# Kernel tuning notes

Measured on AMD Instinct MI355X. Metric: run time of the kernel, lower is better.

The kernel has to match this reference:

```python
import jax, jax.numpy as jnp
import numpy as np

GRID_MIN, GRID_MAX, GRID_SIZE = -4.0, 4.0, 12
BANDWIDTH = (GRID_MAX - GRID_MIN) / max(GRID_SIZE - 1, 1)  # 8/11


def setup_inputs() -> dict:
    key = jax.random.key(0)
    k1, k2, k3, k4 = jax.random.split(key, 4)
    B, I, O, G = 16384, 512, 512, GRID_SIZE
    x = jax.random.normal(k1, (B, I), dtype=jnp.float32)
    coeff = jax.random.normal(k2, (I, O, G), dtype=jnp.float32) * 0.05
    base_w = jax.random.normal(k3, (O, I), dtype=jnp.float32) * (1.0 / np.sqrt(I))
    base_b = jax.random.normal(k4, (O,), dtype=jnp.float32) * 0.01
    centers = jnp.linspace(GRID_MIN, GRID_MAX, G, dtype=jnp.float32)
    return {"x": x, "coeff": coeff, "base_w": base_w, "base_b": base_b, "centers": centers}


def reference(x, coeff, base_w, base_b, centers):
    # RBF basis: [B, I, G]
    diff = (x[..., None] - centers) / jnp.float32(BANDWIDTH)
    basis = jnp.exp(-0.5 * diff * diff)
    # spline contraction over in_dim and grid: [B, O]
    spline = jnp.einsum('big,iog->bo', basis, coeff)
    # residual base linear (torch Linear: x @ W^T + b)
    return spline + x @ base_w.T + base_b
```

## Files before the change

### kernel.cpp

```cpp
#include <hip/hip_runtime.h>
#include <hip/hip_bf16.h>


#define N_DIM 512
#define I_DIM 512
#define KTOT  6656
#define NSTEP 104

typedef short short8 __attribute__((ext_vector_type(8)));
typedef float f32x16 __attribute__((ext_vector_type(16)));
typedef unsigned int u32x4 __attribute__((ext_vector_type(4)));

#define CVTPK(dst, lo, hi) \
  asm("v_cvt_pk_bf16_f32 %0, %1, %2" : "=v"(dst) : "v"(lo), "v"(hi))

__device__ __forceinline__ unsigned short f2bf(float f) {
  union { float f; unsigned int u; } c; c.f = f;
  unsigned int r = (c.u + 0x7FFFu + ((c.u >> 16) & 1)) >> 16;
  return (unsigned short)r;
}

__global__ __launch_bounds__(256) void prep_w(const float* __restrict__ coeff,
                                              const float* __restrict__ base_w,
                                              unsigned short* __restrict__ Wb2) {
  int t = blockIdx.x * 256 + threadIdx.x;
  int e0 = (t & 1) * 4;
  int go = t >> 1;
  int o  = go & 511;
  int g  = go >> 9;
  int k4 = g * 8 + e0;
  int ic = k4 / 832;
  int rem = k4 - ic * 832;
  int slot = rem >> 6;
  int ii = rem & 63;
  int i = ic * 64 + ii;
  float v0, v1, v2, v3;
  if (slot == 0) {
    const float4 bw = *(const float4*)(base_w + (size_t)o * I_DIM + i);
    v0 = bw.x; v1 = bw.y; v2 = bw.z; v3 = bw.w;
  } else {
    int gg = slot - 1;
    const float* cp = coeff + (size_t)i * (N_DIM * 12) + o * 12 + gg;
    v0 = cp[0]; v1 = cp[6144]; v2 = cp[2 * 6144]; v3 = cp[3 * 6144];
  }
  ushort4 s;
  s.x = f2bf(v0); s.y = f2bf(v1); s.z = f2bf(v2); s.w = f2bf(v3);
  *(ushort4*)(Wb2 + (size_t)go * 8 + e0) = s;
}

__global__ __launch_bounds__(512, 2) void kan_gemm(const float* __restrict__ x,
                                                   const unsigned short* __restrict__ Wb2,
                                                   const float* __restrict__ bias,
                                                   float* __restrict__ out) {
  __shared__ unsigned short Asw[4 * 8 * 128 * 8];

  const int tid  = threadIdx.x;
  const int lane = tid & 63;
  const int wid  = tid >> 6;
  const int wm   = wid >> 2, wn = wid & 3;
  const int l31  = lane & 31, hl = lane >> 5;

  const int bid = blockIdx.x;
  const int xcd = bid & 7, jj = bid >> 3;
  const int cb  = xcd >> 2;
  const int rb  = jj * 4 + (xcd & 3);
  const int M0  = rb * 128;
  const int N0  = cb * 256;

  const int arow = tid & 127;
  const int kgp  = tid >> 7;
  const float* xg = x + (size_t)(M0 + arow) * I_DIM + kgp * 16;
  const int aoff0 = ((kgp * 2) * 128 + arow) * 16;
  const int aoff1 = ((kgp * 2 + 1) * 128 + arow) * 16;

  const char* Wb = (const char*)Wb2;
  int boff[4][2];
#pragma unroll
  for (int s = 0; s < 4; ++s)
#pragma unroll
    for (int fo = 0; fo < 2; ++fo)
      boff[s][fo] = (((s * 2 + hl) * 512) + N0 + wn * 64 + fo * 32 + l31) * 16;

  const int aBase = (hl * 128 + wm * 64 + l31) * 16;

  f32x16 acc[2][2];
#pragma unroll
  for (int i = 0; i < 2; ++i)
#pragma unroll
    for (int j = 0; j < 2; ++j)
#pragma unroll
      for (int r = 0; r < 16; ++r) acc[i][j][r] = 0.f;

  float bb[16], ff[16];
  float4 xh[4];
  int eslot = 0, cchunk = 0;
#pragma unroll
  for (int q = 0; q < 4; ++q) xh[q] = *(const float4*)(xg + q * 4);

  auto loadB = [&](short8 (&bv)[4][2], int tt) {
    const char* WbT = Wb + (size_t)tt * 65536;
#pragma unroll
    for (int s = 0; s < 4; ++s) {
      bv[s][0] = *(const short8*)(WbT + boff[s][0]);
      bv[s][1] = *(const short8*)(WbT + boff[s][1]);
    }
  };

  auto emitA = [&](char* pDst) {
    unsigned int w[8];
    if (eslot == 0) {
      float f[16];
#pragma unroll
      for (int q = 0; q < 4; ++q) {
        f[q*4+0] = xh[q].x; f[q*4+1] = xh[q].y; f[q*4+2] = xh[q].z; f[q*4+3] = xh[q].w;
      }
#pragma unroll
      for (int j = 0; j < 8; ++j) CVTPK(w[j], f[2*j], f[2*j+1]);
      *(u32x4*)(pDst + aoff0) = (u32x4){w[0], w[1], w[2], w[3]};
      *(u32x4*)(pDst + aoff1) = (u32x4){w[4], w[5], w[6], w[7]};
#pragma unroll
      for (int j = 0; j < 16; ++j) {
        float u = fmaf(f[j], 1.375f, 5.5f);
        bb[j] = exp2f(-0.72134752044448170f * u * u);
        ff[j] = exp2f(fmaf(u, 1.44269504088896340f, -0.72134752044448170f));
      }
    } else {
#pragma unroll
      for (int j = 0; j < 8; ++j) CVTPK(w[j], bb[2*j], bb[2*j+1]);
      *(u32x4*)(pDst + aoff0) = (u32x4){w[0], w[1], w[2], w[3]};
      *(u32x4*)(pDst + aoff1) = (u32x4){w[4], w[5], w[6], w[7]};
#pragma unroll
      for (int j = 0; j < 16; ++j) {
        bb[j] *= ff[j];
        ff[j] *= 0.36787944117144233f;
      }
    }
    if (eslot == 1 && cchunk < 7) {
      ++cchunk;
      const float* xn = xg + (size_t)cchunk * 64;
#pragma unroll
      for (int q = 0; q < 4; ++q) xh[q] = *(const float4*)(xn + q * 4);
    }
    eslot = (eslot == 12) ? 0 : eslot + 1;
  };

#define MFMA_CLUSTER(AV, BV)                                                         \
  _Pragma("unroll")                                                                  \
  for (int s = 0; s < 4; ++s) {                                                      \
    acc[0][0] = __builtin_amdgcn_mfma_f32_32x32x16_bf16(AV[s][0], BV[s][0], acc[0][0], 0, 0, 0); \
    acc[0][1] = __builtin_amdgcn_mfma_f32_32x32x16_bf16(AV[s][0], BV[s][1], acc[0][1], 0, 0, 0); \
    acc[1][0] = __builtin_amdgcn_mfma_f32_32x32x16_bf16(AV[s][1], BV[s][0], acc[1][0], 0, 0, 0); \
    acc[1][1] = __builtin_amdgcn_mfma_f32_32x32x16_bf16(AV[s][1], BV[s][1], acc[1][1], 0, 0, 0); \
  }

  auto stepBody = [&](int tt, int rdOff, int emOff,
                      short8 (&bvC)[4][2], short8 (&bvN)[4][2]) {
    if (tt < NSTEP - 1) loadB(bvN, tt + 1);
    const char* pA = (const char*)Asw + rdOff;
    short8 av[4][2];
#pragma unroll
    for (int s = 0; s < 4; ++s) {
      av[s][0] = *(const short8*)(pA + aBase + s * 4096);
      av[s][1] = *(const short8*)(pA + aBase + s * 4096 + 512);
    }
    if (tt < NSTEP - 2) emitA((char*)Asw + emOff);
    MFMA_CLUSTER(av, bvC);
  };

  short8 bvA[4][2], bvB[4][2];
  emitA((char*)Asw);
  emitA((char*)Asw + 16384);
  loadB(bvA, 0);
  asm volatile("s_waitcnt lgkmcnt(0)" ::: "memory");
  __builtin_amdgcn_s_barrier();

#pragma unroll 1
  for (int t = 0; t < NSTEP; t += 4) {
    stepBody(t,     0,     32768, bvA, bvB);
    stepBody(t + 1, 16384, 49152, bvB, bvA);
    asm volatile("s_waitcnt lgkmcnt(0)" ::: "memory");
    __builtin_amdgcn_s_barrier();
    stepBody(t + 2, 32768, 0,     bvA, bvB);
    stepBody(t + 3, 49152, 16384, bvB, bvA);
    asm volatile("s_waitcnt lgkmcnt(0)" ::: "memory");
    __builtin_amdgcn_s_barrier();
  }

  float bvv[2];
#pragma unroll
  for (int fo = 0; fo < 2; ++fo) bvv[fo] = bias[N0 + wn * 64 + fo * 32 + l31];
  const int rbase = 4 * hl;
#pragma unroll
  for (int fb = 0; fb < 2; ++fb) {
#pragma unroll
    for (int fo = 0; fo < 2; ++fo) {
      const size_t cix = (size_t)(N0 + wn * 64 + fo * 32 + l31);
#pragma unroll
      for (int r = 0; r < 16; ++r) {
        int row = M0 + wm * 64 + fb * 32 + (r & 3) + 8 * (r >> 2) + rbase;
        out[(size_t)row * N_DIM + cix] = acc[fb][fo][r] + bvv[fo];
      }
    }
  }
}

extern "C" void kernel_launch(void* const* d_in, const int* in_sizes, int n_in,
                              void* d_out, int out_size, void* d_ws, size_t ws_size,
                              hipStream_t stream) {
  const float* x      = (const float*)d_in[0];
  const float* coeff  = (const float*)d_in[1];
  const float* base_w = (const float*)d_in[2];
  const float* base_b = (const float*)d_in[3];
  unsigned short* Wb2 = (unsigned short*)d_ws;

  prep_w<<<3328, 256, 0, stream>>>(coeff, base_w, Wb2);
  kan_gemm<<<256, 512, 0, stream>>>(x, Wb2, base_b, (float*)d_out);
}
```

Measured before the change: 132.6 us.

## Warp-specialize GEMM into producer waves for RBF basis and consumer MFMA waves

Splits the eight waves per block into four producer waves, which compute the bf16 x and RBF basis tiles into a four-deep LDS ring, and four consumer waves, which run the MFMAs over all 128 rows with a 64-column slice each. The K step is halved to 32 (208 steps), so the weight-prep layout and the LDS footprint change to match. The intent is to overlap the exp-heavy basis generation with tensor-core work instead of interleaving both in every wave. The cost is that only half the waves issue MFMAs, there are twice as many barriers, and consumer waves hold more accumulators.

```diff
diff --git a/kernel.cpp b/kernel.cpp
--- a/kernel.cpp
+++ b/kernel.cpp
@@ -5,7 +5,7 @@
 #define N_DIM 512
 #define I_DIM 512
 #define KTOT  6656
-#define NSTEP 104
+#define NSTEP 208
 
 typedef short short8 __attribute__((ext_vector_type(8)));
 typedef float f32x16 __attribute__((ext_vector_type(16)));
@@ -29,11 +29,11 @@
   int o  = go & 511;
   int g  = go >> 9;
   int k4 = g * 8 + e0;
-  int ic = k4 / 832;
-  int rem = k4 - ic * 832;
-  int slot = rem >> 6;
-  int ii = rem & 63;
-  int i = ic * 64 + ii;
+  int ic = k4 / 416;
+  int rem = k4 - ic * 416;
+  int slot = rem >> 5;
+  int ii = rem & 31;
+  int i = ic * 32 + ii;
   float v0, v1, v2, v3;
   if (slot == 0) {
     const float4 bw = *(const float4*)(base_w + (size_t)o * I_DIM + i);
@@ -52,13 +52,13 @@
                                                    const unsigned short* __restrict__ Wb2,
                                                    const float* __restrict__ bias,
                                                    float* __restrict__ out) {
-  __shared__ unsigned short Asw[4 * 8 * 128 * 8];
+  __shared__ unsigned short Asw[4 * 4 * 128 * 8];
 
   const int tid  = threadIdx.x;
   const int lane = tid & 63;
   const int wid  = tid >> 6;
-  const int wm   = wid >> 2, wn = wid & 3;
   const int l31  = lane & 31, hl = lane >> 5;
+  const bool isCons = (wid >= 4);
 
   const int bid = blockIdx.x;
   const int xcd = bid & 7, jj = bid >> 3;
@@ -67,57 +67,31 @@
   const int M0  = rb * 128;
   const int N0  = cb * 256;
 
-  const int arow = tid & 127;
-  const int kgp  = tid >> 7;
-  const float* xg = x + (size_t)(M0 + arow) * I_DIM + kgp * 16;
-  const int aoff0 = ((kgp * 2) * 128 + arow) * 16;
-  const int aoff1 = ((kgp * 2 + 1) * 128 + arow) * 16;
-
   const char* Wb = (const char*)Wb2;
-  int boff[4][2];
-#pragma unroll
-  for (int s = 0; s < 4; ++s)
-#pragma unroll
-    for (int fo = 0; fo < 2; ++fo)
-      boff[s][fo] = (((s * 2 + hl) * 512) + N0 + wn * 64 + fo * 32 + l31) * 16;
-
-  const int aBase = (hl * 128 + wm * 64 + l31) * 16;
-
-  f32x16 acc[2][2];
-#pragma unroll
-  for (int i = 0; i < 2; ++i)
-#pragma unroll
-    for (int j = 0; j < 2; ++j)
-#pragma unroll
-      for (int r = 0; r < 16; ++r) acc[i][j][r] = 0.f;
-
+
+  const int pid  = (wid & 3) * 64 + lane;
+  const int prow = pid & 127;
+  const int pkh  = pid >> 7;
+  const float* xrow = x + (size_t)(M0 + prow) * I_DIM + pkh * 16;
+  const int paoff0 = ((pkh * 2) * 128 + prow) * 16;
+  const int paoff1 = ((pkh * 2 + 1) * 128 + prow) * 16;
   float bb[16], ff[16];
-  float4 xh[4];
-  int eslot = 0, cchunk = 0;
-#pragma unroll
-  for (int q = 0; q < 4; ++q) xh[q] = *(const float4*)(xg + q * 4);
-
-  auto loadB = [&](short8 (&bv)[4][2], int tt) {
-    const char* WbT = Wb + (size_t)tt * 65536;
-#pragma unroll
-    for (int s = 0; s < 4; ++s) {
-      bv[s][0] = *(const short8*)(WbT + boff[s][0]);
-      bv[s][1] = *(const short8*)(WbT + boff[s][1]);
-    }
-  };
-
-  auto emitA = [&](char* pDst) {
+  int eslot = 0, echunk = 0;
+
+  auto emitP = [&](char* pDst) {
     unsigned int w[8];
     if (eslot == 0) {
-      float f[16];
-#pragma unroll
-      for (int q = 0; q < 4; ++q) {
-        f[q*4+0] = xh[q].x; f[q*4+1] = xh[q].y; f[q*4+2] = xh[q].z; f[q*4+3] = xh[q].w;
-      }
+      const float* xp = xrow + echunk * 32;
+      float4 p0 = *(const float4*)(xp);
+      float4 p1 = *(const float4*)(xp + 4);
+      float4 p2 = *(const float4*)(xp + 8);
+      float4 p3 = *(const float4*)(xp + 12);
+      float f[16] = {p0.x,p0.y,p0.z,p0.w, p1.x,p1.y,p1.z,p1.w,
+                     p2.x,p2.y,p2.z,p2.w, p3.x,p3.y,p3.z,p3.w};
 #pragma unroll
       for (int j = 0; j < 8; ++j) CVTPK(w[j], f[2*j], f[2*j+1]);
-      *(u32x4*)(pDst + aoff0) = (u32x4){w[0], w[1], w[2], w[3]};
-      *(u32x4*)(pDst + aoff1) = (u32x4){w[4], w[5], w[6], w[7]};
+      *(u32x4*)(pDst + paoff0) = (u32x4){w[0], w[1], w[2], w[3]};
+      *(u32x4*)(pDst + paoff1) = (u32x4){w[4], w[5], w[6], w[7]};
 #pragma unroll
       for (int j = 0; j < 16; ++j) {
         float u = fmaf(f[j], 1.375f, 5.5f);
@@ -127,78 +101,101 @@
     } else {
 #pragma unroll
       for (int j = 0; j < 8; ++j) CVTPK(w[j], bb[2*j], bb[2*j+1]);
-      *(u32x4*)(pDst + aoff0) = (u32x4){w[0], w[1], w[2], w[3]};
-      *(u32x4*)(pDst + aoff1) = (u32x4){w[4], w[5], w[6], w[7]};
+      *(u32x4*)(pDst + paoff0) = (u32x4){w[0], w[1], w[2], w[3]};
+      *(u32x4*)(pDst + paoff1) = (u32x4){w[4], w[5], w[6], w[7]};
 #pragma unroll
       for (int j = 0; j < 16; ++j) {
         bb[j] *= ff[j];
         ff[j] *= 0.36787944117144233f;
       }
     }
-    if (eslot == 1 && cchunk < 7) {
-      ++cchunk;
-      const float* xn = xg + (size_t)cchunk * 64;
-#pragma unroll
-      for (int q = 0; q < 4; ++q) xh[q] = *(const float4*)(xn + q * 4);
-    }
-    eslot = (eslot == 12) ? 0 : eslot + 1;
+    if (eslot == 12) { eslot = 0; ++echunk; } else { ++eslot; }
   };
 
-#define MFMA_CLUSTER(AV, BV)                                                         \
-  _Pragma("unroll")                                                                  \
-  for (int s = 0; s < 4; ++s) {                                                      \
-    acc[0][0] = __builtin_amdgcn_mfma_f32_32x32x16_bf16(AV[s][0], BV[s][0], acc[0][0], 0, 0, 0); \
-    acc[0][1] = __builtin_amdgcn_mfma_f32_32x32x16_bf16(AV[s][0], BV[s][1], acc[0][1], 0, 0, 0); \
-    acc[1][0] = __builtin_amdgcn_mfma_f32_32x32x16_bf16(AV[s][1], BV[s][0], acc[1][0], 0, 0, 0); \
-    acc[1][1] = __builtin_amdgcn_mfma_f32_32x32x16_bf16(AV[s][1], BV[s][1], acc[1][1], 0, 0, 0); \
-  }
-
-  auto stepBody = [&](int tt, int rdOff, int emOff,
-                      short8 (&bvC)[4][2], short8 (&bvN)[4][2]) {
-    if (tt < NSTEP - 1) loadB(bvN, tt + 1);
-    const char* pA = (const char*)Asw + rdOff;
-    short8 av[4][2];
-#pragma unroll
-    for (int s = 0; s < 4; ++s) {
-      av[s][0] = *(const short8*)(pA + aBase + s * 4096);
-      av[s][1] = *(const short8*)(pA + aBase + s * 4096 + 512);
-    }
-    if (tt < NSTEP - 2) emitA((char*)Asw + emOff);
-    MFMA_CLUSTER(av, bvC);
+  const int cw = (wid & 3);
+  int boff[2][2];
+#pragma unroll
+  for (int s = 0; s < 2; ++s)
+#pragma unroll
+    for (int fo = 0; fo < 2; ++fo)
+      boff[s][fo] = (((s * 2 + hl) * 512) + N0 + cw * 64 + fo * 32 + l31) * 16;
+  const int aBase = hl * 2048 + l31 * 16;
+
+  f32x16 acc[4][2];
+#pragma unroll
+  for (int i = 0; i < 4; ++i)
+#pragma unroll
+    for (int j = 0; j < 2; ++j)
+#pragma unroll
+      for (int r = 0; r < 16; ++r) acc[i][j][r] = 0.f;
+
+  short8 bv[2][2];
+
+  auto loadBnext = [&](int tt) {
+    const char* WbT = Wb + (size_t)tt * 32768;
+#pragma unroll
+    for (int s = 0; s < 2; ++s) {
+      bv[s][0] = *(const short8*)(WbT + boff[s][0]);
+      bv[s][1] = *(const short8*)(WbT + boff[s][1]);
+    }
   };
 
-  short8 bvA[4][2], bvB[4][2];
-  emitA((char*)Asw);
-  emitA((char*)Asw + 16384);
-  loadB(bvA, 0);
+  auto consStep = [&](int tt, bool loadNext) {
+    const char* pA = (const char*)Asw + ((tt & 3) << 13);
+#pragma unroll
+    for (int s = 0; s < 2; ++s) {
+      short8 av[4];
+#pragma unroll
+      for (int fb = 0; fb < 4; ++fb)
+        av[fb] = *(const short8*)(pA + s * 4096 + fb * 512 + aBase);
+#pragma unroll
+      for (int fb = 0; fb < 4; ++fb) {
+        acc[fb][0] = __builtin_amdgcn_mfma_f32_32x32x16_bf16(av[fb], bv[s][0], acc[fb][0], 0, 0, 0);
+        acc[fb][1] = __builtin_amdgcn_mfma_f32_32x32x16_bf16(av[fb], bv[s][1], acc[fb][1], 0, 0, 0);
+      }
+    }
+    if (loadNext) loadBnext(tt + 1);
+  };
+
+  if (isCons) {
+    loadBnext(0);
+  } else {
+    emitP((char*)Asw);
+    emitP((char*)Asw + 8192);
+  }
   asm volatile("s_waitcnt lgkmcnt(0)" ::: "memory");
   __builtin_amdgcn_s_barrier();
 
 #pragma unroll 1
-  for (int t = 0; t < NSTEP; t += 4) {
-    stepBody(t,     0,     32768, bvA, bvB);
-    stepBody(t + 1, 16384, 49152, bvB, bvA);
+  for (int t = 0; t < 206; t += 2) {
+    if (isCons) {
+      consStep(t, true);
+      consStep(t + 1, true);
+    } else {
+      emitP((char*)Asw + (((t + 2) & 3) << 13));
+      emitP((char*)Asw + (((t + 3) & 3) << 13));
+    }
     asm volatile("s_waitcnt lgkmcnt(0)" ::: "memory");
     __builtin_amdgcn_s_barrier();
-    stepBody(t + 2, 32768, 0,     bvA, bvB);
-    stepBody(t + 3, 49152, 16384, bvB, bvA);
-    asm volatile("s_waitcnt lgkmcnt(0)" ::: "memory");
-    __builtin_amdgcn_s_barrier();
-  }
-
-  float bvv[2];
-#pragma unroll
-  for (int fo = 0; fo < 2; ++fo) bvv[fo] = bias[N0 + wn * 64 + fo * 32 + l31];
-  const int rbase = 4 * hl;
-#pragma unroll
-  for (int fb = 0; fb < 2; ++fb) {
-#pragma unroll
-    for (int fo = 0; fo < 2; ++fo) {
-      const size_t cix = (size_t)(N0 + wn * 64 + fo * 32 + l31);
-#pragma unroll
-      for (int r = 0; r < 16; ++r) {
-        int row = M0 + wm * 64 + fb * 32 + (r & 3) + 8 * (r >> 2) + rbase;
-        out[(size_t)row * N_DIM + cix] = acc[fb][fo][r] + bvv[fo];
+  }
+  if (isCons) {
+    consStep(206, true);
+    consStep(207, false);
+
+    float bvv[2];
+#pragma unroll
+    for (int fo = 0; fo < 2; ++fo) bvv[fo] = bias[N0 + cw * 64 + fo * 32 + l31];
+    const int rbase = 4 * hl;
+#pragma unroll
+    for (int fb = 0; fb < 4; ++fb) {
+#pragma unroll
+      for (int fo = 0; fo < 2; ++fo) {
+        const size_t cix = (size_t)(N0 + cw * 64 + fo * 32 + l31);
+#pragma unroll
+        for (int r = 0; r < 16; ++r) {
+          int row = M0 + fb * 32 + (r & 3) + 8 * (r >> 2) + rbase;
+          out[(size_t)row * N_DIM + cix] = acc[fb][fo][r] + bvv[fo];
+        }
       }
     }
   }
```

Result: slower. 168.2 us (+26.9%).
